# Optimization experiments

Hardware: AMD Instinct MI355X
Metric: run time of the kernel (lower is better)

Reference implementation:

```python
import jax, jax.numpy as jnp
import numpy as np

B, L, H, NH, NB = 4, 200, 256, 4, 2
HS = H // NH
NEG = -(2.0 ** 32) + 1.0  # torch uses (-2**32 + 1) as mask fill
EPS = 1e-8


def _ln(x, g, b):
    m = x.mean(-1, keepdims=True)
    v = ((x - m) ** 2).mean(-1, keepdims=True)
    return (x - m) / jnp.sqrt(v + EPS) * g + b


def _split_heads(x):  # [B,L,H] -> (NH,B,L,HS), matches torch split(dim=2)+cat(dim=0)
    return x.reshape(x.shape[0], x.shape[1], NH, HS).transpose(2, 0, 1, 3)


def _split_heads4(x):  # [B,L,L,H] -> (NH,B,L,L,HS)
    return x.reshape(B, L, L, NH, HS).transpose(3, 0, 1, 2, 4)


def setup_inputs() -> dict:
    key = jax.random.key(0)
    ks = jax.random.split(key, 20)
    w = 0.05
    inp = {
        "log_seqs": jax.random.randint(ks[0], (B, L), 0, 50000),
        "time_matrices": jax.random.randint(ks[1], (B, L, L), 0, 257),
        "dis_matrices": jax.random.randint(ks[2], (B, L, L), 0, 257),
        "item_embs": jax.random.normal(ks[3], (50001, H), jnp.float32) * w,
        "pos_K_tab": jax.random.normal(ks[4], (L, H), jnp.float32) * w,
        "pos_V_tab": jax.random.normal(ks[5], (L, H), jnp.float32) * w,
        "time_K_tab": jax.random.normal(ks[6], (257, H), jnp.float32) * w,
        "time_V_tab": jax.random.normal(ks[7], (257, H), jnp.float32) * w,
        "dis_K_tab": jax.random.normal(ks[8], (257, H), jnp.float32) * w,
        "dis_V_tab": jax.random.normal(ks[9], (257, H), jnp.float32) * w,
        "ln1_g": jnp.ones((NB, H), jnp.float32),
        "ln1_b": jnp.zeros((NB, H), jnp.float32),
        "Wq": jax.random.normal(ks[10], (NB, H, H), jnp.float32) * w,
        "bq": jnp.zeros((NB, H), jnp.float32),
        "Wk": jax.random.normal(ks[11], (NB, H, H), jnp.float32) * w,
        "bk": jnp.zeros((NB, H), jnp.float32),
        "Wv": jax.random.normal(ks[12], (NB, H, H), jnp.float32) * w,
        "bv": jnp.zeros((NB, H), jnp.float32),
        "ln2_g": jnp.ones((NB, H), jnp.float32),
        "ln2_b": jnp.zeros((NB, H), jnp.float32),
        "W1": jax.random.normal(ks[13], (NB, H, H), jnp.float32) * w,
        "b1": jnp.zeros((NB, H), jnp.float32),
        "W2": jax.random.normal(ks[14], (NB, H, H), jnp.float32) * w,
        "b2": jnp.zeros((NB, H), jnp.float32),
        "lnf_g": jnp.ones((H,), jnp.float32),
        "lnf_b": jnp.zeros((H,), jnp.float32),
    }
    return inp


def _seq2feats(log_seqs, time_matrices, dis_matrices, item_embs,
               pos_K_tab, pos_V_tab, time_K_tab, time_V_tab, dis_K_tab, dis_V_tab,
               ln1_g, ln1_b, Wq, bq, Wk, bk, Wv, bv,
               ln2_g, ln2_b, W1, b1, W2, b2, lnf_g, lnf_b):
    # embedded relative matrices: (NH,B,L,L,HS)
    tK = _split_heads4(time_K_tab[time_matrices])
    tV = _split_heads4(time_V_tab[time_matrices])
    dK = _split_heads4(dis_K_tab[dis_matrices])
    dV = _split_heads4(dis_V_tab[dis_matrices])
    pK = pos_K_tab.reshape(L, NH, HS).transpose(1, 0, 2)  # (NH,L,HS), same for every batch row
    pV = pos_V_tab.reshape(L, NH, HS).transpose(1, 0, 2)

    pad = (log_seqs == 0)  # [B,L]
    keep = (~pad)[..., None].astype(jnp.float32)
    seqs = item_embs[log_seqs] * keep

    causal = ~jnp.tril(jnp.ones((L, L), dtype=bool))  # strictly upper
    mask = pad[None, :, :, None] | causal[None, None, :, :]  # (1,B,L,L) broadcast over heads
    scale = jnp.sqrt(jnp.float32(HS))

    for i in range(NB):
        Qn = _ln(seqs, ln1_g[i], ln1_b[i])
        Qh = _split_heads(Qn @ Wq[i].T + bq[i])
        Kh = _split_heads(seqs @ Wk[i].T + bk[i])
        Vh = _split_heads(seqs @ Wv[i].T + bv[i])
        s = (jnp.einsum('hbqd,hbkd->hbqk', Qh, Kh)
             + jnp.einsum('hbqd,hkd->hbqk', Qh, pK)
             + jnp.einsum('hbqkd,hbqd->hbqk', tK, Qh)
             + jnp.einsum('hbqkd,hbqd->hbqk', dK, Qh)) / scale
        s = jnp.where(mask, NEG, s)
        A = jax.nn.softmax(s, axis=-1)  # (NH,B,L,L)
        o = (jnp.einsum('hbqk,hbkd->hbqd', A, Vh)
             + jnp.einsum('hbqk,hkd->hbqd', A, pV)
             + jnp.einsum('hbqk,hbqkd->hbqd', A, tV)
             + jnp.einsum('hbqk,hbqkd->hbqd', A, dV))
        mha = o.transpose(1, 2, 0, 3).reshape(B, L, H)
        seqs = Qn + mha
        x = _ln(seqs, ln2_g[i], ln2_b[i])
        h = jax.nn.relu(x @ W1[i].T + b1[i])  # Conv1d k=1 == pointwise linear
        seqs = (h @ W2[i].T + b2[i]) + x
        seqs = seqs * keep
    return _ln(seqs, lnf_g, lnf_b)


def reference(log_seqs, time_matrices, dis_matrices, item_embs,
              pos_K_tab, pos_V_tab, time_K_tab, time_V_tab, dis_K_tab, dis_V_tab,
              ln1_g, ln1_b, Wq, bq, Wk, bk, Wv, bv,
              ln2_g, ln2_b, W1, b1, W2, b2, lnf_g, lnf_b):
    return _seq2feats(log_seqs, time_matrices, dis_matrices, item_embs,
                      pos_K_tab, pos_V_tab, time_K_tab, time_V_tab, dis_K_tab, dis_V_tab,
                      ln1_g, ln1_b, Wq, bq, Wk, bk, Wv, bv,
                      ln2_g, ln2_b, W1, b1, W2, b2, lnf_g, lnf_b)
```

## Files before the change

### kernel.cpp

```cpp
#include <hip/hip_runtime.h>
#include <math.h>

typedef __fp16 h2 __attribute__((ext_vector_type(2)));
typedef __fp16 f16x8 __attribute__((ext_vector_type(8)));
typedef float f32x4 __attribute__((ext_vector_type(4)));

#define Bc 4
#define Lc 200
#define Hc 256
#define NHc 4
#define HSc 64
#define NBc 2
#define Mtot (Bc*Lc)
#define LDH 264
#define WN (2*Hc*Hc)
#define TN (257*Hc)

static __device__ __forceinline__ float neg_fill() { return -4294967295.0f; }
static __device__ __forceinline__ int rl(int x) { return __builtin_amdgcn_readfirstlane(x); }

static __device__ __forceinline__ uint pkh2(float a, float b) {
  h2 r = __builtin_amdgcn_cvt_pkrtz(a, b);
  return __builtin_bit_cast(uint, r);
}
static __device__ __forceinline__ h2 u2h(uint u) { return __builtin_bit_cast(h2, u); }
static __device__ __forceinline__ float h2f(ushort u) {
  return (float)__builtin_bit_cast(_Float16, u);
}

__global__ void cvtw_k(const float* __restrict__ Wq, const float* __restrict__ Wk,
                       const float* __restrict__ Wv, const float* __restrict__ W1,
                       const float* __restrict__ W2,
                       const float* __restrict__ tK, const float* __restrict__ tV,
                       const float* __restrict__ dK, const float* __restrict__ dV,
                       ushort* __restrict__ out) {
  int y = blockIdx.y;
  const float* src;
  int n, off;
  if (y < 5) {
    n = WN; off = y * WN;
    src = (y == 0) ? Wq : (y == 1) ? Wk : (y == 2) ? Wv : (y == 3) ? W1 : W2;
  } else {
    n = TN; off = 5 * WN + (y - 5) * TN;
    src = (y == 5) ? tK : (y == 6) ? tV : (y == 7) ? dK : dV;
  }
  int idx = (blockIdx.x * 256 + threadIdx.x) * 8;
  if (idx >= n) return;
  float4 a = *(const float4*)&src[idx];
  float4 b = *(const float4*)&src[idx + 4];
  uint4 o;
  o.x = pkh2(a.x, a.y); o.y = pkh2(a.z, a.w);
  o.z = pkh2(b.x, b.y); o.w = pkh2(b.z, b.w);
  *(uint4*)&out[off + idx] = o;
}

__global__ __launch_bounds__(256)
void mmqkv_k(const float* __restrict__ seqs, const float* __restrict__ emb,
             const int* __restrict__ logs, int useEmb,
             const float* __restrict__ g, const float* __restrict__ bt,
             const ushort* __restrict__ Wq16, const ushort* __restrict__ Wk16,
             const ushort* __restrict__ Wv16,
             const float* __restrict__ bq, const float* __restrict__ bk,
             const float* __restrict__ bv,
             const float* __restrict__ pK, const float* __restrict__ pV,
             float* __restrict__ Qn,
             ushort* __restrict__ Q16, ushort* __restrict__ K16,
             ushort* __restrict__ V16) {
  __shared__ __fp16 Al[16][LDH];
  __shared__ __fp16 Wl[64][LDH];
  int m0 = blockIdx.x * 16;
  int y = blockIdx.y;
  int region = y >> 2, nloc = (y & 3) * 64;
  const ushort* Wsrc = (region == 0) ? Wq16 : (region == 1 ? Wk16 : Wv16);
  const float* bias = (region == 0) ? bq : (region == 1 ? bk : bv);
  int t = threadIdx.x;
  if (region == 0) {
    int r = t >> 4, c0 = (t & 15) * 16;
    int m = m0 + r;
    const float* xr;
    bool zero = false;
    if (useEmb) {
      int tok = logs[m];
      zero = (tok == 0);
      xr = &emb[tok * Hc + c0];
    } else {
      xr = &seqs[m * Hc + c0];
    }
    float4 v0, v1, v2, v3;
    if (zero) {
      v0 = v1 = v2 = v3 = make_float4(0.f, 0.f, 0.f, 0.f);
    } else {
      v0 = *(const float4*)&xr[0];
      v1 = *(const float4*)&xr[4];
      v2 = *(const float4*)&xr[8];
      v3 = *(const float4*)&xr[12];
    }
    float s = v0.x + v0.y + v0.z + v0.w + v1.x + v1.y + v1.z + v1.w
            + v2.x + v2.y + v2.z + v2.w + v3.x + v3.y + v3.z + v3.w;
    float q = v0.x*v0.x + v0.y*v0.y + v0.z*v0.z + v0.w*v0.w
            + v1.x*v1.x + v1.y*v1.y + v1.z*v1.z + v1.w*v1.w
            + v2.x*v2.x + v2.y*v2.y + v2.z*v2.z + v2.w*v2.w
            + v3.x*v3.x + v3.y*v3.y + v3.z*v3.z + v3.w*v3.w;
#pragma unroll
    for (int o = 1; o < 16; o <<= 1) { s += __shfl_xor(s, o); q += __shfl_xor(q, o); }
    float mean = s * (1.f / Hc);
    float var = q * (1.f / Hc) - mean * mean;
    float rstd = 1.f / sqrtf(var + 1e-8f);
    float tmp[16] = {v0.x,v0.y,v0.z,v0.w,v1.x,v1.y,v1.z,v1.w,
                     v2.x,v2.y,v2.z,v2.w,v3.x,v3.y,v3.z,v3.w};
    float nv[16];
#pragma unroll
    for (int j = 0; j < 16; ++j)
      nv[j] = (tmp[j] - mean) * rstd * g[c0 + j] + bt[c0 + j];
#pragma unroll
    for (int j = 0; j < 16; j += 2)
      *(h2*)&Al[r][c0 + j] = __builtin_amdgcn_cvt_pkrtz(nv[j], nv[j + 1]);
    if (y == 0) {
#pragma unroll
      for (int j = 0; j < 16; j += 4)
        *(float4*)&Qn[m * Hc + c0 + j] = make_float4(nv[j], nv[j+1], nv[j+2], nv[j+3]);
    }
  } else {
    for (int i = t; i < 16 * 64; i += 256) {
      int r = i >> 6, c = (i & 63) * 4;
      int m = m0 + r;
      float4 v;
      if (useEmb) {
        int tok = logs[m];
        v = (tok == 0) ? make_float4(0.f, 0.f, 0.f, 0.f)
                       : *(const float4*)&emb[tok * Hc + c];
      } else {
        v = *(const float4*)&seqs[m * Hc + c];
      }
      *(h2*)&Al[r][c] = __builtin_amdgcn_cvt_pkrtz(v.x, v.y);
      *(h2*)&Al[r][c + 2] = __builtin_amdgcn_cvt_pkrtz(v.z, v.w);
    }
  }
  for (int i = t; i < 2048; i += 256) {
    int r = i >> 5, c = (i & 31) * 8;
    uint4 v = *(const uint4*)&Wsrc[(nloc + r) * Hc + c];
    *(uint4*)&Wl[r][c] = v;
  }
  __syncthreads();
  int wave = t >> 6, lane = t & 63;
  int row = lane & 15, kg = lane >> 4;
  int bn = wave * 16 + row;
  f32x4 acc = {0.f, 0.f, 0.f, 0.f};
#pragma unroll
  for (int k0 = 0; k0 < Hc; k0 += 32) {
    int kk = k0 + kg * 8;
    f16x8 a = *(const f16x8*)&Al[row][kk];
    f16x8 bb = *(const f16x8*)&Wl[bn][kk];
    acc = __builtin_amdgcn_mfma_f32_16x16x32_f16(a, bb, acc, 0, 0, 0);
  }
  int coln = nloc + wave * 16 + row;
  ushort* op = (region == 0) ? Q16 : (region == 1 ? K16 : V16);
  const float* pT = (region == 1) ? pK : pV;
#pragma unroll
  for (int r = 0; r < 4; ++r) {
    int m = m0 + kg * 4 + r;
    float v = acc[r] + bias[coln];
    if (region) v += pT[(m % Lc) * Hc + coln];
    op[m * Hc + coln] = __builtin_bit_cast(ushort, (_Float16)v);
  }
}

__global__ __launch_bounds__(1024, 8)
void attn_k(const ushort* __restrict__ Q16, const ushort* __restrict__ K16,
            const ushort* __restrict__ V16,
            const ushort* __restrict__ tK16, const ushort* __restrict__ dK16,
            const ushort* __restrict__ tV16, const ushort* __restrict__ dV16,
            const int* __restrict__ tm, const int* __restrict__ dm,
            const int* __restrict__ logs,
            const float* __restrict__ Qn, float* __restrict__ seqs) {
  int h = blockIdx.x, b = blockIdx.y, bz = blockIdx.z;
  __shared__ float S0l[16][212];
  __shared__ float Tql[16][272];
  __shared__ float Dql[16][272];
  __shared__ float sArow[16][204];
  int t = threadIdx.x;
  int wave = t >> 6, lane = t & 63;
  int row16 = lane & 15, kg = lane >> 4;
  {
    int qa = row16 * 16 + bz;
    bool va = qa < Lc;
    f16x8 A0 = {0,0,0,0,0,0,0,0}, A1 = A0;
    if (va) {
      const ushort* Qr = &Q16[(b * Lc + qa) * Hc + h * HSc];
      A0 = *(const f16x8*)&Qr[kg * 8];
      A1 = *(const f16x8*)&Qr[32 + kg * 8];
    }
    for (int j = wave; j < 47; j += 16) {
      int kind, n;
      if (j < 13) { kind = 0; n = j; }
      else if (j < 30) { kind = 1; n = j - 13; }
      else { kind = 2; n = j - 30; }
      int col = n * 16 + row16;
      const ushort* Bsrc;
      bool vb;
      if (kind == 0) { vb = col < Lc; Bsrc = &K16[(b * Lc + (vb ? col : 0)) * Hc + h * HSc]; }
      else { vb = col < 257; Bsrc = &((kind == 1) ? tK16 : dK16)[(vb ? col : 0) * Hc + h * HSc]; }
      f16x8 B0 = {0,0,0,0,0,0,0,0}, B1 = B0;
      if (vb) {
        B0 = *(const f16x8*)&Bsrc[kg * 8];
        B1 = *(const f16x8*)&Bsrc[32 + kg * 8];
      }
      f32x4 acc = {0.f, 0.f, 0.f, 0.f};
      acc = __builtin_amdgcn_mfma_f32_16x16x32_f16(A0, B0, acc, 0, 0, 0);
      acc = __builtin_amdgcn_mfma_f32_16x16x32_f16(A1, B1, acc, 0, 0, 0);
      if (kind == 0) {
#pragma unroll
        for (int r = 0; r < 4; ++r) S0l[kg * 4 + r][col] = acc[r];
      } else if (kind == 1) {
#pragma unroll
        for (int r = 0; r < 4; ++r) Tql[kg * 4 + r][col] = acc[r];
      } else {
#pragma unroll
        for (int r = 0; r < 4; ++r) Dql[kg * 4 + r][col] = acc[r];
      }
    }
  }
  __syncthreads();
  int q = wave * 16 + bz;
  if (q >= Lc) return;
  int m = b * Lc + q;
  int oi = m * Hc + h * HSc + lane;
  if (logs[m] == 0) { seqs[oi] = Qn[oi]; return; }
  const int* tmr = tm + rl(m * Lc);
  const int* dmr = dm + rl(m * Lc);
  const float* srow = S0l[wave];
  const float* trow = Tql[wave];
  const float* drow = Dql[wave];
  int np = (q >> 6) + 1;
  float sv[4];
  float mx = neg_fill();
#pragma unroll
  for (int p = 0; p < 4; ++p) {
    sv[p] = neg_fill();
    if (p >= np) continue;
    int k = p * 64 + lane;
    int kc = (k <= q) ? k : q;
    int ti = tmr[kc], di = dmr[kc];
    float sc = (srow[kc] + trow[ti] + drow[di]) * 0.125f;
    if (k <= q) sv[p] = sc;
    mx = fmaxf(mx, sv[p]);
  }
#pragma unroll
  for (int o = 32; o; o >>= 1) mx = fmaxf(mx, __shfl_xor(mx, o));
  float sum = 0.f;
  float ev[4];
#pragma unroll
  for (int p = 0; p < 4; ++p) {
    ev[p] = __expf(sv[p] - mx);
    sum += ev[p];
  }
#pragma unroll
  for (int o = 32; o; o >>= 1) sum += __shfl_xor(sum, o);
  float rs = 1.f / sum;
#pragma unroll
  for (int p = 0; p < 4; ++p) {
    if (p >= np) continue;
    int k = p * 64 + lane;
    if (k < Lc) sArow[wave][k] = ev[p] * rs;
  }
  for (int k = q + 1 + lane; k < 204; k += 64) sArow[wave][k] = 0.f;
  int half = lane >> 5, li = lane & 31;
  const uint* Vu  = (const uint*)V16 + rl(b * Lc * (Hc / 2) + h * (HSc / 2)) + li;
  const uint* tVg = (const uint*)tV16 + rl(h * (HSc / 2)) + li;
  const uint* dVg = (const uint*)dV16 + rl(h * (HSc / 2)) + li;
  float acc0 = 0.f, acc1 = 0.f, acc2 = 0.f, acc3 = 0.f;
  for (int k0 = 0; k0 <= q; k0 += 4) {
    int ka = k0 + half;
    int kb = k0 + 2 + half;
    int kca = (ka <= q) ? ka : q;
    int kcb = (kb <= q) ? kb : q;
    float aa = sArow[wave][ka];
    float ab = sArow[wave][kb];
    int ti0 = tmr[kca], di0 = dmr[kca];
    int ti1 = tmr[kcb], di1 = dmr[kcb];
    uint tv0 = tVg[ti0 * (Hc / 2)];
    uint dv0 = dVg[di0 * (Hc / 2)];
    uint vv0 = Vu[kca * (Hc / 2)];
    uint tv1 = tVg[ti1 * (Hc / 2)];
    uint dv1 = dVg[di1 * (Hc / 2)];
    uint vv1 = Vu[kcb * (Hc / 2)];
    h2 s0 = u2h(tv0) + u2h(dv0) + u2h(vv0);
    h2 s1 = u2h(tv1) + u2h(dv1) + u2h(vv1);
    acc0 = fmaf(aa, (float)s0.x, acc0);
    acc1 = fmaf(aa, (float)s0.y, acc1);
    acc2 = fmaf(ab, (float)s1.x, acc2);
    acc3 = fmaf(ab, (float)s1.y, acc3);
  }
  float accLo = acc0 + acc2; accLo += __shfl_xor(accLo, 32);
  float accHi = acc1 + acc3; accHi += __shfl_xor(accHi, 32);
  if (half == 0) {
    int oib = m * Hc + h * HSc + 2 * li;
    float2 qv = *(const float2*)&Qn[oib];
    float2 r;
    r.x = qv.x + accLo;
    r.y = qv.y + accHi;
    *(float2*)&seqs[oib] = r;
  }
}

template <int FIN>
__global__ __launch_bounds__(512)
void ffn_k(float* __restrict__ seqs,
           const float* __restrict__ g, const float* __restrict__ bt,
           const ushort* __restrict__ W1_16, const float* __restrict__ b1,
           const ushort* __restrict__ W2_16, const float* __restrict__ b2,
           const int* __restrict__ logs,
           const float* __restrict__ lnf_g, const float* __restrict__ lnf_b,
           float* __restrict__ dout) {
  __shared__ __fp16 Xl[16][LDH];
  __shared__ __fp16 Hl[16][LDH];
  __shared__ __fp16 Wl[128][LDH];
  __shared__ float Ol[16][Hc];
  int m0 = blockIdx.x * 16;
  int t = threadIdx.x;
  {
    int r = t >> 5, c0 = (t & 31) * 8;
    const float* xr = &seqs[(m0 + r) * Hc + c0];
    float4 v0 = *(const float4*)&xr[0];
    float4 v1 = *(const float4*)&xr[4];
    float s = v0.x + v0.y + v0.z + v0.w + v1.x + v1.y + v1.z + v1.w;
    float q = v0.x*v0.x + v0.y*v0.y + v0.z*v0.z + v0.w*v0.w
            + v1.x*v1.x + v1.y*v1.y + v1.z*v1.z + v1.w*v1.w;
#pragma unroll
    for (int o = 1; o < 32; o <<= 1) { s += __shfl_xor(s, o); q += __shfl_xor(q, o); }
    float mean = s * (1.f / Hc);
    float var = q * (1.f / Hc) - mean * mean;
    float rstd = 1.f / sqrtf(var + 1e-8f);
    float tmp[8] = {v0.x,v0.y,v0.z,v0.w,v1.x,v1.y,v1.z,v1.w};
    float nv[8];
#pragma unroll
    for (int j = 0; j < 8; ++j)
      nv[j] = (tmp[j] - mean) * rstd * g[c0 + j] + bt[c0 + j];
#pragma unroll
    for (int j = 0; j < 8; j += 2)
      *(h2*)&Xl[r][c0 + j] = __builtin_amdgcn_cvt_pkrtz(nv[j], nv[j + 1]);
  }
  int wave = t >> 6, lane = t & 63;
  int row = lane & 15, kg = lane >> 4;
#pragma unroll
  for (int ch = 0; ch < 2; ++ch) {
    __syncthreads();
    for (int i = t; i < 4096; i += 512) {
      int r = i >> 5, c = (i & 31) * 8;
      uint4 v = *(const uint4*)&W1_16[(ch * 128 + r) * Hc + c];
      *(uint4*)&Wl[r][c] = v;
    }
    __syncthreads();
    int bn = wave * 16 + row;
    f32x4 acc = {0.f, 0.f, 0.f, 0.f};
#pragma unroll
    for (int k0 = 0; k0 < Hc; k0 += 32) {
      int kk = k0 + kg * 8;
      f16x8 a = *(const f16x8*)&Xl[row][kk];
      f16x8 bb = *(const f16x8*)&Wl[bn][kk];
      acc = __builtin_amdgcn_mfma_f32_16x16x32_f16(a, bb, acc, 0, 0, 0);
    }
    int coln = ch * 128 + wave * 16 + row;
    float bv = b1[coln];
#pragma unroll
    for (int r = 0; r < 4; ++r) {
      float v = fmaxf(acc[r] + bv, 0.f);
      Hl[kg * 4 + r][coln] = (_Float16)v;
    }
  }
#pragma unroll
  for (int ch = 0; ch < 2; ++ch) {
    __syncthreads();
    for (int i = t; i < 4096; i += 512) {
      int r = i >> 5, c = (i & 31) * 8;
      uint4 v = *(const uint4*)&W2_16[(ch * 128 + r) * Hc + c];
      *(uint4*)&Wl[r][c] = v;
    }
    __syncthreads();
    int bn = wave * 16 + row;
    f32x4 acc = {0.f, 0.f, 0.f, 0.f};
#pragma unroll
    for (int k0 = 0; k0 < Hc; k0 += 32) {
      int kk = k0 + kg * 8;
      f16x8 a = *(const f16x8*)&Hl[row][kk];
      f16x8 bb = *(const f16x8*)&Wl[bn][kk];
      acc = __builtin_amdgcn_mfma_f32_16x16x32_f16(a, bb, acc, 0, 0, 0);
    }
    int coln = ch * 128 + wave * 16 + row;
    float bv = b2[coln];
#pragma unroll
    for (int r = 0; r < 4; ++r) {
      int mrow = kg * 4 + r;
      int m = m0 + mrow;
      float keep = (logs[m] != 0) ? 1.f : 0.f;
      float xv = h2f(__builtin_bit_cast(ushort, Xl[mrow][coln]));
      float val = (acc[r] + bv + xv) * keep;
      if (FIN) Ol[mrow][coln] = val;
      else     seqs[m * Hc + coln] = val;
    }
  }
  if (FIN) {
    __syncthreads();
    int r = t >> 5, c0 = (t & 31) * 8;
    float v[8];
#pragma unroll
    for (int j = 0; j < 8; ++j) v[j] = Ol[r][c0 + j];
    float s = 0.f, q = 0.f;
#pragma unroll
    for (int j = 0; j < 8; ++j) { s += v[j]; q += v[j] * v[j]; }
#pragma unroll
    for (int o = 1; o < 32; o <<= 1) { s += __shfl_xor(s, o); q += __shfl_xor(q, o); }
    float mean = s * (1.f / Hc);
    float var = q * (1.f / Hc) - mean * mean;
    float rstd = 1.f / sqrtf(var + 1e-8f);
#pragma unroll
    for (int j = 0; j < 8; ++j)
      dout[(m0 + r) * Hc + c0 + j] = (v[j] - mean) * rstd * lnf_g[c0 + j] + lnf_b[c0 + j];
  }
}

extern "C" void kernel_launch(void* const* d_in, const int* in_sizes, int n_in,
                              void* d_out, int out_size, void* d_ws, size_t ws_size,
                              hipStream_t stream) {
  const int* logs = (const int*)d_in[0];
  const int* tm   = (const int*)d_in[1];
  const int* dm   = (const int*)d_in[2];
  const float* item = (const float*)d_in[3];
  const float* pK = (const float*)d_in[4];
  const float* pV = (const float*)d_in[5];
  const float* tK = (const float*)d_in[6];
  const float* tV = (const float*)d_in[7];
  const float* dK = (const float*)d_in[8];
  const float* dV = (const float*)d_in[9];
  const float* ln1_g = (const float*)d_in[10];
  const float* ln1_b = (const float*)d_in[11];
  const float* Wq = (const float*)d_in[12];
  const float* bq = (const float*)d_in[13];
  const float* Wk = (const float*)d_in[14];
  const float* bk = (const float*)d_in[15];
  const float* Wv = (const float*)d_in[16];
  const float* bv = (const float*)d_in[17];
  const float* ln2_g = (const float*)d_in[18];
  const float* ln2_b = (const float*)d_in[19];
  const float* W1 = (const float*)d_in[20];
  const float* b1 = (const float*)d_in[21];
  const float* W2 = (const float*)d_in[22];
  const float* b2 = (const float*)d_in[23];
  const float* lnf_g = (const float*)d_in[24];
  const float* lnf_b = (const float*)d_in[25];

  const int NROW = Mtot * Hc;
  float* ws = (float*)d_ws;
  float* sSeqs = ws + 0 * NROW;
  float* sQn   = ws + 1 * NROW;
  ushort* Q16  = (ushort*)(ws + 2 * NROW);
  ushort* K16  = Q16 + NROW;
  ushort* V16  = K16 + NROW;
  ushort* w16  = (ushort*)(ws + 4 * NROW);
  ushort* wq16 = w16 + 0 * WN;
  ushort* wk16 = w16 + 1 * WN;
  ushort* wv16 = w16 + 2 * WN;
  ushort* w116 = w16 + 3 * WN;
  ushort* w216 = w16 + 4 * WN;
  ushort* tK16 = w16 + 5 * WN;
  ushort* tV16 = tK16 + TN;
  ushort* dK16 = tV16 + TN;
  ushort* dV16 = dK16 + TN;

  dim3 gC(64, 9);
  cvtw_k<<<gC, 256, 0, stream>>>(Wq, Wk, Wv, W1, W2, tK, tV, dK, dV, w16);

  dim3 gQKV(Mtot / 16, 12);
  dim3 ga(NHc, Bc, 16);
  const int HHh = Hc * Hc;
  for (int i = 0; i < NBc; ++i) {
    mmqkv_k<<<gQKV, 256, 0, stream>>>(sSeqs, item, logs, (i == 0) ? 1 : 0,
                                      ln1_g + i * Hc, ln1_b + i * Hc,
                                      wq16 + i * HHh, wk16 + i * HHh, wv16 + i * HHh,
                                      bq + i * Hc, bk + i * Hc, bv + i * Hc,
                                      pK, pV, sQn, Q16, K16, V16);
    attn_k<<<ga, 1024, 0, stream>>>(Q16, K16, V16,
                                    tK16, dK16, tV16, dV16,
                                    tm, dm, logs, sQn, sSeqs);
    if (i == 0)
      ffn_k<0><<<Mtot / 16, 512, 0, stream>>>(sSeqs, ln2_g + i * Hc, ln2_b + i * Hc,
                                              w116 + i * HHh, b1 + i * Hc,
                                              w216 + i * HHh, b2 + i * Hc, logs,
                                              nullptr, nullptr, nullptr);
    else
      ffn_k<1><<<Mtot / 16, 512, 0, stream>>>(sSeqs, ln2_g + i * Hc, ln2_b + i * Hc,
                                              w116 + i * HHh, b1 + i * Hc,
                                              w216 + i * HHh, b2 + i * Hc, logs,
                                              lnf_g, lnf_b, (float*)d_out);
  }
}
```

Before: 81.25 us.

## Replace per-key V gather with binned probabilities and MFMA against transposed tables

The attention output no longer walks keys one at a time, gathering V, time-V and distance-V rows. Each query's softmax weights are scatter-added with LDS atomics into per-index bins for the time and distance tables. Three MFMA products then run: probabilities against a transposed V, and the two bin vectors against transposed, padded tV/dV tables. The V projection now writes V transposed, the conversion kernel builds the transposed tables, and launch bounds are relaxed. This trades the latency-bound serial gather for tensor-core work plus LDS atomics and fp16 rounding of weights. The padding columns of Vt are never written, so uninitialized workspace could leak NaNs into the result.

```diff
diff --git a/kernel.cpp b/kernel.cpp
--- a/kernel.cpp
+++ b/kernel.cpp
@@ -15,6 +15,8 @@
 #define LDH 264
 #define WN (2*Hc*Hc)
 #define TN (257*Hc)
+#define TTW 288
+#define VTW 224
 
 static __device__ __forceinline__ float neg_fill() { return -4294967295.0f; }
 static __device__ __forceinline__ int rl(int x) { return __builtin_amdgcn_readfirstlane(x); }
@@ -35,6 +37,22 @@
                        const float* __restrict__ dK, const float* __restrict__ dV,
                        ushort* __restrict__ out) {
   int y = blockIdx.y;
+  if (y >= 9) {
+    const float* srcT = (y == 9) ? tV : dV;
+    ushort* dst = out + 5 * WN + 4 * TN + (y - 9) * (Hc * TTW);
+    int idx = (blockIdx.x * 256 + threadIdx.x) * 8;
+    if (idx >= Hc * TTW) return;
+    int hd = idx / TTW, c0 = idx % TTW;
+    ushort v[8];
+#pragma unroll
+    for (int j = 0; j < 8; ++j) {
+      int c = c0 + j;
+      float f = (c < 257) ? srcT[c * Hc + hd] : 0.f;
+      v[j] = __builtin_bit_cast(ushort, (_Float16)f);
+    }
+    *(uint4*)&dst[idx] = *(uint4*)v;
+    return;
+  }
   const float* src;
   int n, off;
   if (y < 5) {
@@ -65,7 +83,7 @@
              const float* __restrict__ pK, const float* __restrict__ pV,
              float* __restrict__ Qn,
              ushort* __restrict__ Q16, ushort* __restrict__ K16,
-             ushort* __restrict__ V16) {
+             ushort* __restrict__ Vt) {
   __shared__ __fp16 Al[16][LDH];
   __shared__ __fp16 Wl[64][LDH];
   int m0 = blockIdx.x * 16;
@@ -154,22 +172,36 @@
     acc = __builtin_amdgcn_mfma_f32_16x16x32_f16(a, bb, acc, 0, 0, 0);
   }
   int coln = nloc + wave * 16 + row;
-  ushort* op = (region == 0) ? Q16 : (region == 1 ? K16 : V16);
-  const float* pT = (region == 1) ? pK : pV;
-#pragma unroll
-  for (int r = 0; r < 4; ++r) {
-    int m = m0 + kg * 4 + r;
-    float v = acc[r] + bias[coln];
-    if (region) v += pT[(m % Lc) * Hc + coln];
-    op[m * Hc + coln] = __builtin_bit_cast(ushort, (_Float16)v);
-  }
-}
-
-__global__ __launch_bounds__(1024, 8)
+  float bcol = bias[coln];
+  if (region == 2) {
+    int mbase = m0 + kg * 4;
+    int b2 = mbase / Lc;
+    int q0 = mbase - b2 * Lc;
+    float v0 = acc[0] + bcol + pV[(q0 + 0) * Hc + coln];
+    float v1 = acc[1] + bcol + pV[(q0 + 1) * Hc + coln];
+    float v2 = acc[2] + bcol + pV[(q0 + 2) * Hc + coln];
+    float v3 = acc[3] + bcol + pV[(q0 + 3) * Hc + coln];
+    uint2 pk;
+    pk.x = pkh2(v0, v1);
+    pk.y = pkh2(v2, v3);
+    *(uint2*)&Vt[((size_t)(b2 * Hc + coln)) * VTW + q0] = pk;
+  } else {
+    ushort* op = (region == 0) ? Q16 : K16;
+#pragma unroll
+    for (int r = 0; r < 4; ++r) {
+      int m = m0 + kg * 4 + r;
+      float v = acc[r] + bcol;
+      if (region) v += pK[(m % Lc) * Hc + coln];
+      op[m * Hc + coln] = __builtin_bit_cast(ushort, (_Float16)v);
+    }
+  }
+}
+
+__global__ __launch_bounds__(1024, 4)
 void attn_k(const ushort* __restrict__ Q16, const ushort* __restrict__ K16,
-            const ushort* __restrict__ V16,
+            const ushort* __restrict__ Vt,
             const ushort* __restrict__ tK16, const ushort* __restrict__ dK16,
-            const ushort* __restrict__ tV16, const ushort* __restrict__ dV16,
+            const ushort* __restrict__ tVt, const ushort* __restrict__ dVt,
             const int* __restrict__ tm, const int* __restrict__ dm,
             const int* __restrict__ logs,
             const float* __restrict__ Qn, float* __restrict__ seqs) {
@@ -177,10 +209,19 @@
   __shared__ float S0l[16][212];
   __shared__ float Tql[16][272];
   __shared__ float Dql[16][272];
-  __shared__ float sArow[16][204];
+  __shared__ __fp16 A16[16][296];
+  __shared__ float binsT[16][264];
+  __shared__ float binsD[16][264];
+  __shared__ __fp16 Wt16[16][296];
+  __shared__ __fp16 Wd16[16][296];
+  __shared__ float Opart[3][16][64];
   int t = threadIdx.x;
   int wave = t >> 6, lane = t & 63;
   int row16 = lane & 15, kg = lane >> 4;
+  for (int i = t; i < 16 * 264; i += 1024) {
+    (&binsT[0][0])[i] = 0.f;
+    (&binsD[0][0])[i] = 0.f;
+  }
   {
     int qa = row16 * 16 + bz;
     bool va = qa < Lc;
@@ -222,84 +263,89 @@
   }
   __syncthreads();
   int q = wave * 16 + bz;
-  if (q >= Lc) return;
   int m = b * Lc + q;
-  int oi = m * Hc + h * HSc + lane;
-  if (logs[m] == 0) { seqs[oi] = Qn[oi]; return; }
-  const int* tmr = tm + rl(m * Lc);
-  const int* dmr = dm + rl(m * Lc);
-  const float* srow = S0l[wave];
-  const float* trow = Tql[wave];
-  const float* drow = Dql[wave];
-  int np = (q >> 6) + 1;
-  float sv[4];
-  float mx = neg_fill();
-#pragma unroll
-  for (int p = 0; p < 4; ++p) {
-    sv[p] = neg_fill();
-    if (p >= np) continue;
-    int k = p * 64 + lane;
-    int kc = (k <= q) ? k : q;
-    int ti = tmr[kc], di = dmr[kc];
-    float sc = (srow[kc] + trow[ti] + drow[di]) * 0.125f;
-    if (k <= q) sv[p] = sc;
-    mx = fmaxf(mx, sv[p]);
-  }
-#pragma unroll
-  for (int o = 32; o; o >>= 1) mx = fmaxf(mx, __shfl_xor(mx, o));
-  float sum = 0.f;
-  float ev[4];
-#pragma unroll
-  for (int p = 0; p < 4; ++p) {
-    ev[p] = __expf(sv[p] - mx);
-    sum += ev[p];
-  }
-#pragma unroll
-  for (int o = 32; o; o >>= 1) sum += __shfl_xor(sum, o);
-  float rs = 1.f / sum;
-#pragma unroll
-  for (int p = 0; p < 4; ++p) {
-    if (p >= np) continue;
-    int k = p * 64 + lane;
-    if (k < Lc) sArow[wave][k] = ev[p] * rs;
-  }
-  for (int k = q + 1 + lane; k < 204; k += 64) sArow[wave][k] = 0.f;
-  int half = lane >> 5, li = lane & 31;
-  const uint* Vu  = (const uint*)V16 + rl(b * Lc * (Hc / 2) + h * (HSc / 2)) + li;
-  const uint* tVg = (const uint*)tV16 + rl(h * (HSc / 2)) + li;
-  const uint* dVg = (const uint*)dV16 + rl(h * (HSc / 2)) + li;
-  float acc0 = 0.f, acc1 = 0.f, acc2 = 0.f, acc3 = 0.f;
-  for (int k0 = 0; k0 <= q; k0 += 4) {
-    int ka = k0 + half;
-    int kb = k0 + 2 + half;
-    int kca = (ka <= q) ? ka : q;
-    int kcb = (kb <= q) ? kb : q;
-    float aa = sArow[wave][ka];
-    float ab = sArow[wave][kb];
-    int ti0 = tmr[kca], di0 = dmr[kca];
-    int ti1 = tmr[kcb], di1 = dmr[kcb];
-    uint tv0 = tVg[ti0 * (Hc / 2)];
-    uint dv0 = dVg[di0 * (Hc / 2)];
-    uint vv0 = Vu[kca * (Hc / 2)];
-    uint tv1 = tVg[ti1 * (Hc / 2)];
-    uint dv1 = dVg[di1 * (Hc / 2)];
-    uint vv1 = Vu[kcb * (Hc / 2)];
-    h2 s0 = u2h(tv0) + u2h(dv0) + u2h(vv0);
-    h2 s1 = u2h(tv1) + u2h(dv1) + u2h(vv1);
-    acc0 = fmaf(aa, (float)s0.x, acc0);
-    acc1 = fmaf(aa, (float)s0.y, acc1);
-    acc2 = fmaf(ab, (float)s1.x, acc2);
-    acc3 = fmaf(ab, (float)s1.y, acc3);
-  }
-  float accLo = acc0 + acc2; accLo += __shfl_xor(accLo, 32);
-  float accHi = acc1 + acc3; accHi += __shfl_xor(accHi, 32);
-  if (half == 0) {
-    int oib = m * Hc + h * HSc + 2 * li;
-    float2 qv = *(const float2*)&Qn[oib];
-    float2 r;
-    r.x = qv.x + accLo;
-    r.y = qv.y + accHi;
-    *(float2*)&seqs[oib] = r;
+  bool valid = false;
+  if (q < Lc) valid = (logs[m] != 0);
+  if (valid) {
+    const int* tmr = tm + rl(m * Lc);
+    const int* dmr = dm + rl(m * Lc);
+    const float* srow = S0l[wave];
+    const float* trow = Tql[wave];
+    const float* drow = Dql[wave];
+    int np = (q >> 6) + 1;
+    float sv[4];
+    float mx = neg_fill();
+#pragma unroll
+    for (int p = 0; p < 4; ++p) {
+      sv[p] = neg_fill();
+      if (p >= np) continue;
+      int k = p * 64 + lane;
+      int kc = (k <= q) ? k : q;
+      int ti = tmr[kc], di = dmr[kc];
+      float sc = (srow[kc] + trow[ti] + drow[di]) * 0.125f;
+      if (k <= q) sv[p] = sc;
+      mx = fmaxf(mx, sv[p]);
+    }
+#pragma unroll
+    for (int o = 32; o; o >>= 1) mx = fmaxf(mx, __shfl_xor(mx, o));
+    float sum = 0.f;
+    float ev[4];
+#pragma unroll
+    for (int p = 0; p < 4; ++p) {
+      ev[p] = __expf(sv[p] - mx);
+      sum += ev[p];
+    }
+#pragma unroll
+    for (int o = 32; o; o >>= 1) sum += __shfl_xor(sum, o);
+    float rs = 1.f / sum;
+#pragma unroll
+    for (int p = 0; p < 4; ++p) {
+      int k = p * 64 + lane;
+      float a = ev[p] * rs;
+      A16[wave][k] = (_Float16)a;
+      if (k <= q) {
+        atomicAdd(&binsT[wave][tmr[k]], a);
+        atomicAdd(&binsD[wave][dmr[k]], a);
+      }
+    }
+    for (int k2 = 256 + lane; k2 < 296; k2 += 64) A16[wave][k2] = (_Float16)0.f;
+  } else {
+    for (int k2 = lane; k2 < 296; k2 += 64) A16[wave][k2] = (_Float16)0.f;
+  }
+  for (int c = lane; c < 296; c += 64) {
+    float tv = (c < 264) ? binsT[wave][c] : 0.f;
+    float dv = (c < 264) ? binsD[wave][c] : 0.f;
+    Wt16[wave][c] = (_Float16)tv;
+    Wd16[wave][c] = (_Float16)dv;
+  }
+  __syncthreads();
+  if (wave < 12) {
+    int mat = wave >> 2, ntile = wave & 3;
+    int col = ntile * 16 + row16;
+    const __fp16* Arow = (mat == 0) ? &A16[row16][0]
+                        : (mat == 1) ? &Wt16[row16][0] : &Wd16[row16][0];
+    const ushort* Bp;
+    int nsteps;
+    if (mat == 0) { Bp = Vt + (size_t)(b * Hc + h * HSc + col) * VTW; nsteps = 7; }
+    else {
+      const ushort* Tb = (mat == 1) ? tVt : dVt;
+      Bp = Tb + (size_t)(h * HSc + col) * TTW; nsteps = 9;
+    }
+    f32x4 acc = {0.f, 0.f, 0.f, 0.f};
+    for (int s = 0; s < nsteps; ++s) {
+      int kk = s * 32 + kg * 8;
+      f16x8 a = *(const f16x8*)&Arow[kk];
+      f16x8 bb = *(const f16x8*)&Bp[kk];
+      acc = __builtin_amdgcn_mfma_f32_16x16x32_f16(a, bb, acc, 0, 0, 0);
+    }
+#pragma unroll
+    for (int r = 0; r < 4; ++r) Opart[mat][kg * 4 + r][col] = acc[r];
+  }
+  __syncthreads();
+  if (q < Lc) {
+    int oi = m * Hc + h * HSc + lane;
+    float o = Opart[0][wave][lane] + Opart[1][wave][lane] + Opart[2][wave][lane];
+    seqs[oi] = Qn[oi] + o;
   }
 }
 
@@ -455,7 +501,6 @@
   float* sQn   = ws + 1 * NROW;
   ushort* Q16  = (ushort*)(ws + 2 * NROW);
   ushort* K16  = Q16 + NROW;
-  ushort* V16  = K16 + NROW;
   ushort* w16  = (ushort*)(ws + 4 * NROW);
   ushort* wq16 = w16 + 0 * WN;
   ushort* wk16 = w16 + 1 * WN;
@@ -466,8 +511,11 @@
   ushort* tV16 = tK16 + TN;
   ushort* dK16 = tV16 + TN;
   ushort* dV16 = dK16 + TN;
-
-  dim3 gC(64, 9);
+  ushort* tVt  = dV16 + TN;
+  ushort* dVt  = tVt + Hc * TTW;
+  ushort* Vt   = dVt + Hc * TTW;
+
+  dim3 gC(64, 11);
   cvtw_k<<<gC, 256, 0, stream>>>(Wq, Wk, Wv, W1, W2, tK, tV, dK, dV, w16);
 
   dim3 gQKV(Mtot / 16, 12);
@@ -478,9 +526,9 @@
                                       ln1_g + i * Hc, ln1_b + i * Hc,
                                       wq16 + i * HHh, wk16 + i * HHh, wv16 + i * HHh,
                                       bq + i * Hc, bk + i * Hc, bv + i * Hc,
-                                      pK, pV, sQn, Q16, K16, V16);
-    attn_k<<<ga, 1024, 0, stream>>>(Q16, K16, V16,
-                                    tK16, dK16, tV16, dV16,
+                                      pK, pV, sQn, Q16, K16, Vt);
+    attn_k<<<ga, 1024, 0, stream>>>(Q16, K16, Vt,
+                                    tK16, dK16, tVt, dVt,
                                     tm, dm, logs, sQn, sSeqs);
     if (i == 0)
       ffn_k<0><<<Mtot / 16, 512, 0, stream>>>(sSeqs, ln2_g + i * Hc, ln2_b + i * Hc,
```

New measurement: 69.09 us, median of 2. 1.18x faster.
